# Kernel tuning notes

Hardware: AMD Instinct MI355X
Metric: run time of the kernel (lower is better)

Reference implementation:

```python
import jax, jax.numpy as jnp
import numpy as np

P = 10          # num_patches
EPS = 1e-20
ALPHAS = dict(stretch=1.0, E=1.0, G=1.0, skew=1.0, total_area=1.0, total_area_mult=1.0)
ALPHA_MC = 1.0
ALPHA_DISTORT = 1.0


def setup_inputs() -> dict:
    key = jax.random.key(0)
    k1, k2, k3, k4 = jax.random.split(key, 4)
    B, N, M = 8, 8192, 2500
    pc_gt = jax.random.normal(k1, (B, N, 3), dtype=jnp.float32)
    pc_pred = jax.random.normal(k2, (B, M, 3), dtype=jnp.float32)
    # first fundamental form (E, F, G); ensure E*G - F^2 > 0 so sqrt is smooth
    u = jax.random.uniform(k3, (B, M, 3), dtype=jnp.float32)
    fff = u * 0.5 + jnp.array([1.0, 0.0, 1.0], dtype=jnp.float32)
    A_gt = jax.random.uniform(k4, (B,), dtype=jnp.float32)
    return {"pc_gt": pc_gt, "pc_pred": pc_pred, "fff": fff, "A_gt": A_gt}


def _forward(pc_gt, pc_pred, fff, A_gt):
    B, M, _ = pc_pred.shape
    spp = M // P

    # ---- Chamfer distance via dense (B, M, N) distance matrix + argmin ----
    diff = pc_pred[:, :, None, :] - pc_gt[:, None, :, :]          # (B, M, N, 3)
    distm = jnp.sqrt(jnp.sum(diff * diff, axis=3))                # (B, M, N)
    inds_p2gt = jnp.argmin(distm, axis=2)                         # (B, M)
    inds_gt2p = jnp.argmin(distm, axis=1)                         # (B, N)
    pc_gt_reg = jnp.take_along_axis(pc_gt, inds_p2gt[..., None], axis=1)   # (B, M, 3)
    pc_p_reg = jnp.take_along_axis(pc_pred, inds_gt2p[..., None], axis=1)  # (B, N, 3)
    d_p2gt = jnp.sum((pc_pred - pc_gt_reg) ** 2, axis=2)
    d_gt2p = jnp.sum((pc_gt - pc_p_reg) ** 2, axis=2)
    L_chd = d_p2gt.mean() + d_gt2p.mean()

    # ---- FFF-based losses ----
    EFG = jnp.transpose(fff.reshape(B, P, spp, 3), (3, 0, 1, 2))  # (3, B, P, spp)
    E, F, G = EFG[0], EFG[1], EFG[2]

    # metric consistency between consecutive frame pairs
    Eh = E.reshape(B // 2, 2, P, spp)
    Fh = F.reshape(B // 2, 2, P, spp)
    Gh = G.reshape(B // 2, 2, P, spp)
    L_mc = ((Eh[:, 0] - Eh[:, 1]) ** 2
            + 2.0 * (Fh[:, 0] - Fh[:, 1]) ** 2
            + (Gh[:, 0] - Gh[:, 1]) ** 2).mean()

    # scaled isometry (collapse) losses
    A2 = jnp.maximum(E * G - F * F, 0.0)                          # (B, P, spp)
    A = jnp.sqrt(A2)
    inv = 1.0 / (A2 + EPS)
    L_stretch = (((E - G) ** 2) * inv).mean() * ALPHAS['stretch']
    L_E = (((E - E.mean()) ** 2) * inv).mean() * ALPHAS['E']
    L_G = (((G - G.mean()) ** 2) * inv).mean() * ALPHAS['G']
    L_F = ((F * F) * inv).mean() * ALPHAS['skew']

    # overlap / total-area loss
    A_tot = A.mean(axis=2).sum(axis=1)                            # (B,)
    L_olap = (jnp.maximum(0.0, A_tot - A_gt * ALPHAS['total_area_mult']) ** 2).mean() * ALPHAS['total_area']

    loss_sciso = L_F + L_E + L_G + L_stretch + L_olap
    loss_tot = L_chd + ALPHA_MC * L_mc + ALPHA_DISTORT * loss_sciso
    return loss_tot


def reference(pc_gt, pc_pred, fff, A_gt):
    return _forward(pc_gt, pc_pred, fff, A_gt)
```

## Files before the change

kernel.cpp:

```cpp
#include <hip/hip_runtime.h>

#define B_   8
#define N_   8192
#define M_   2500
#define SPP_ 250
#define EPS_ 1e-20f
#define BIGF 1e30f

#define NB_P2GT 640
#define NB_GT2P 512
#define NB_FFF  79
#define NB_K1   (NB_P2GT + NB_GT2P + NB_FFF)

#define NB_RG2P 256
#define NB_RP2  79
#define NB_K2   (NB_RG2P + NB_RP2)

#define WS_P2GT 0
#define WS_GT2P 160000
#define WS_F1P  291072
#define WS_RED  292968
#define WS_CNT  293303
#define RO_G2P 0
#define RO_P2  256
#define F_E    0
#define F_G    1
#define F_MC   2
#define F_ST   3
#define F_F2I  4
#define F_E2I  5
#define F_EI   6
#define F_G2I  7
#define F_GI   8
#define F_I    9
#define F_AB   10

typedef __attribute__((ext_vector_type(8))) short short8_t;
typedef __attribute__((ext_vector_type(4))) float float4_t;

__device__ __forceinline__ unsigned pack_bf2(float lo, float hi) {
    unsigned a = __float_as_uint(lo);
    unsigned b = __float_as_uint(hi);
    a = (a + 0x7FFFu + ((a >> 16) & 1u)) >> 16;
    b = (b + 0x7FFFu + ((b >> 16) & 1u)) & 0xFFFF0000u;
    return a | b;
}
__device__ __forceinline__ short bf16s(float x) {
    unsigned a = __float_as_uint(x);
    return (short)((a + 0x7FFFu + ((a >> 16) & 1u)) >> 16);
}
__device__ __forceinline__ float wave_sum64(float v) {
    #pragma unroll
    for (int o = 32; o > 0; o >>= 1) v += __shfl_down(v, o, 64);
    return v;
}
__device__ __forceinline__ float block_sum256(float v, volatile float* red4) {
    v = wave_sum64(v);
    int wid = threadIdx.x >> 6, lane = threadIdx.x & 63;
    if (lane == 0) red4[wid] = v;
    __syncthreads();
    float r = 0.f;
    if (threadIdx.x == 0) r = red4[0] + red4[1] + red4[2] + red4[3];
    __syncthreads();
    return r;
}
__device__ __forceinline__ void min4(float4_t& c, const float4_t d) {
    c.x = fminf(c.x, d.x); c.y = fminf(c.y, d.y);
    c.z = fminf(c.z, d.z); c.w = fminf(c.w, d.w);
}
__device__ __forceinline__ void quad_min4(float4_t& c) {
    #pragma unroll
    for (int m = 1; m < 16; m <<= 1) {
        c.x = fminf(c.x, __shfl_xor(c.x, m, 64));
        c.y = fminf(c.y, __shfl_xor(c.y, m, 64));
        c.z = fminf(c.z, __shfl_xor(c.z, m, 64));
        c.w = fminf(c.w, __shfl_xor(c.w, m, 64));
    }
}

__global__ void __launch_bounds__(256, 4) k1_main(
        const float* __restrict__ gt, const float* __restrict__ pred,
        const float* __restrict__ fff, float* __restrict__ ws) {
    __shared__ uint4 spts[1280];
    __shared__ __align__(16) float saux[264];
    const int bid = blockIdx.x;
    const int tid = threadIdx.x;
    const int lane = tid & 63;
    const int w    = tid >> 6;
    const int quad = lane >> 4;
    const int l15  = lane & 15;

    if (bid == 0 && tid == 0) ((unsigned*)(ws + WS_CNT))[0] = 0u;

    if (bid < NB_P2GT + NB_GT2P) {
        const bool is_p2gt = bid < NB_P2GT;
        int b, mblk, z, ntiles, blim, alim;
        const float* apts; const float* bpts; float* dst;
        if (is_p2gt) {
            z = bid / 80; int rem = bid % 80;
            b = rem / 10; mblk = rem % 10;
            apts = pred + (size_t)b * M_ * 3;
            bpts = gt + ((size_t)b * N_ + (size_t)z * 1024) * 3;
            ntiles = 64; blim = 1024; alim = M_;
            dst = ws + WS_P2GT + (size_t)z * 20000 + b * M_;
        } else {
            int r = bid - NB_P2GT;
            z = r >> 8; int rem = r & 255;
            b = rem >> 5; mblk = rem & 31;
            apts = gt + (size_t)b * N_ * 3;
            bpts = pred + ((size_t)b * M_ + (size_t)z * 1280) * 3;
            ntiles = 80; blim = M_ - z * 1280; alim = N_;
            dst = ws + WS_GT2P + (size_t)z * 65536 + b * N_;
        }
        const int abase = mblk * 256;
        const int nstage = ntiles * 16;

        for (int i = tid; i < nstage; i += 256) {
            float x = 0.f, y = 0.f, zc = 0.f, n2 = BIGF;
            if (i < blim) {
                x = bpts[i * 3 + 0]; y = bpts[i * 3 + 1]; zc = bpts[i * 3 + 2];
                n2 = x * x + y * y + zc * zc;
            }
            uint4 q;
            q.x = pack_bf2(-2.f * x, -2.f * y);
            q.y = pack_bf2(-2.f * zc, n2);
            q.z = q.x; q.w = q.y;
            spts[i] = q;
        }

        short8_t af[4];
        #pragma unroll
        for (int t = 0; t < 4; ++t) af[t] = (short8_t){0,0,0,0,0,0,0,0};
        if (lane < 16) {
            #pragma unroll
            for (int t = 0; t < 4; ++t) {
                int m = abase + w * 64 + t * 16 + l15;
                int c = m < alim ? m : alim - 1;
                float x = apts[c*3+0], y = apts[c*3+1], zc = apts[c*3+2];
                af[t][0] = bf16s(x); af[t][1] = bf16s(y); af[t][2] = bf16s(zc);
                af[t][3] = (short)0x3F80;
                saux[w * 64 + t * 16 + l15] = x*x + y*y + zc*zc;
            }
        }
        __syncthreads();

        const float4_t* bp = (const float4_t*)saux;
        float4_t bias[4], c[4];
        #pragma unroll
        for (int t = 0; t < 4; ++t) {
            bias[t] = bp[w * 16 + t * 4 + quad];
            c[t] = (float4_t){BIGF, BIGF, BIGF, BIGF};
        }

        const uint4* bptr = spts + l15;
        const int npairs = ntiles >> 1;
        #pragma unroll 2
        for (int i = 0; i < npairs; ++i) {
            short8_t bf0 = __builtin_bit_cast(short8_t, bptr[(2*i)   * 16]);
            short8_t bf1 = __builtin_bit_cast(short8_t, bptr[(2*i+1) * 16]);
            #pragma unroll
            for (int t = 0; t < 4; ++t) {
                float4_t d = __builtin_amdgcn_mfma_f32_16x16x32_bf16(
                                 af[t], bf0, bias[t], 0, 0, 0);
                min4(c[t], d);
            }
            #pragma unroll
            for (int t = 0; t < 4; ++t) {
                float4_t d = __builtin_amdgcn_mfma_f32_16x16x32_bf16(
                                 af[t], bf1, bias[t], 0, 0, 0);
                min4(c[t], d);
            }
        }
        #pragma unroll
        for (int t = 0; t < 4; ++t) {
            quad_min4(c[t]);
            c[t].x = fmaxf(c[t].x, 0.f); c[t].y = fmaxf(c[t].y, 0.f);
            c[t].z = fmaxf(c[t].z, 0.f); c[t].w = fmaxf(c[t].w, 0.f);
        }
        if (l15 == 0) {
            #pragma unroll
            for (int t = 0; t < 4; ++t) {
                int m0 = abase + w * 64 + t * 16 + quad * 4;
                if (m0 < alim)
                    *(float4_t*)(dst + m0) = c[t];
            }
        }
    } else {
        const int kb = bid - NB_P2GT - NB_GT2P;
        const int i  = kb * 256 + tid;
        volatile float* red4 = saux + 256;
        float* sA = saux;
        if (tid < B_) sA[tid] = 0.f;
        __syncthreads();

        float vE=0.f,vG=0.f,vMC=0.f,vST=0.f,vF2=0.f,vE2=0.f,vEI=0.f,
              vG2=0.f,vGI=0.f,vI=0.f;
        if (i < B_ * M_) {
            const int b = i / M_;
            const int m = i - b * M_;
            const float* f = fff + (size_t)i * 3;
            float E = f[0], F = f[1], G = f[2];
            float A2  = fmaxf(E * G - F * F, 0.f);
            float inv = 1.f / (A2 + EPS_);
            vE = E; vG = G;
            vST = (E - G) * (E - G) * inv;
            vF2 = F * F * inv;
            vE2 = E * E * inv; vEI = E * inv;
            vG2 = G * G * inv; vGI = G * inv;
            vI  = inv;
            atomicAdd(&sA[b], sqrtf(A2));
            if ((b & 1) == 0) {
                const float* f2 = fff + ((size_t)(b + 1) * M_ + m) * 3;
                float dE = E - f2[0], dF = F - f2[1], dG = G - f2[2];
                vMC = dE * dE + 2.f * dF * dF + dG * dG;
            }
        }
        float* outp = ws + WS_F1P + (size_t)kb * 24;
        float r;
        r = block_sum256(vE,  red4); if (tid==0) outp[F_E]   = r;
        r = block_sum256(vG,  red4); if (tid==0) outp[F_G]   = r;
        r = block_sum256(vMC, red4); if (tid==0) outp[F_MC]  = r;
        r = block_sum256(vST, red4); if (tid==0) outp[F_ST]  = r;
        r = block_sum256(vF2, red4); if (tid==0) outp[F_F2I] = r;
        r = block_sum256(vE2, red4); if (tid==0) outp[F_E2I] = r;
        r = block_sum256(vEI, red4); if (tid==0) outp[F_EI]  = r;
        r = block_sum256(vG2, red4); if (tid==0) outp[F_G2I] = r;
        r = block_sum256(vGI, red4); if (tid==0) outp[F_GI]  = r;
        r = block_sum256(vI,  red4); if (tid==0) outp[F_I]   = r;
        __syncthreads();
        if (tid < B_) outp[F_AB + tid] = sA[tid];
    }
}

__global__ void __launch_bounds__(256) k2_reduce(
        const float* __restrict__ fff, const float* __restrict__ A_gt,
        float* __restrict__ ws, float* __restrict__ out) {
    __shared__ float red4[4];
    const int bid = blockIdx.x;
    const int tid = threadIdx.x;
    float* redp = ws + WS_RED;
    const float* f1p = ws + WS_F1P;

    if (bid < NB_RG2P) {
        const int o = bid * 256 + tid;
        const float* src = ws + WS_GT2P + o;
        float m = fminf(src[0], src[65536]);
        float r = block_sum256(m, red4);
        if (tid == 0) redp[RO_G2P + bid] = r;
    } else {
        const int kb = bid - NB_RG2P;
        const int o = kb * 256 + tid;
        float s = 0.f;
        if (o < 20000) {
            const float* src = ws + WS_P2GT + o;
            float m = src[0];
            #pragma unroll
            for (int zz = 1; zz < 8; ++zz) m = fminf(m, src[zz * 20000]);
            s = m;
        }
        float r = block_sum256(s, red4);
        if (tid == 0) redp[RO_P2 + kb] = r;
    }

    __syncthreads();
    if (tid == 0) __threadfence();
    __syncthreads();
    __shared__ unsigned old_s;
    if (tid == 0)
        old_s = __hip_atomic_fetch_add((unsigned*)(ws + WS_CNT), 1u,
                                       __ATOMIC_ACQ_REL, __HIP_MEMORY_SCOPE_AGENT);
    __syncthreads();
    if (old_s == (unsigned)(NB_K2 - 1)) {
        float v;
        v = redp[RO_G2P + tid];
        float sGT2P = block_sum256(v, red4);
        v = (tid < 79) ? redp[RO_P2 + tid] : 0.f;
        float sP2GT = block_sum256(v, red4);
        float a[18];
        #pragma unroll
        for (int k = 0; k < 18; ++k) {
            v = (tid < 79) ? f1p[tid * 24 + k] : 0.f;
            a[k] = block_sum256(v, red4);
        }
        if (tid == 0) {
            const float inv20k = 1.f / 20000.f;
            float mE = a[F_E] * inv20k, mG = a[F_G] * inv20k;
            float L_E = (a[F_E2I] - 2.f*mE*a[F_EI] + mE*mE*a[F_I]) * inv20k;
            float L_G = (a[F_G2I] - 2.f*mG*a[F_GI] + mG*mG*a[F_I]) * inv20k;
            float L_sc = L_E + L_G + (a[F_ST] + a[F_F2I]) * inv20k;
            float L_mc = a[F_MC] * (1.f / 10000.f);
            float L_chd = sP2GT * inv20k + sGT2P * (1.f / 65536.f);
            float L_olap = 0.f;
            #pragma unroll
            for (int b = 0; b < B_; ++b) {
                float At = a[F_AB + b] * (1.f / (float)SPP_);
                float d  = fmaxf(0.f, At - A_gt[b]);
                L_olap += d * d;
            }
            L_olap *= (1.f / (float)B_);
            out[0] = L_chd + L_mc + L_sc + L_olap;
        }
    }
}

extern "C" void kernel_launch(void* const* d_in, const int* in_sizes, int n_in,
                              void* d_out, int out_size, void* d_ws, size_t ws_size,
                              hipStream_t stream) {
    const float* pc_gt   = (const float*)d_in[0];
    const float* pc_pred = (const float*)d_in[1];
    const float* fff     = (const float*)d_in[2];
    const float* A_gt    = (const float*)d_in[3];
    float* ws  = (float*)d_ws;
    float* out = (float*)d_out;

    k1_main  <<<NB_K1, 256, 0, stream>>>(pc_gt, pc_pred, fff, ws);
    k2_reduce<<<NB_K2, 256, 0, stream>>>(fff, A_gt, ws, out);
}
```

Measured before the change: 100.9 us.

## Enlarge Chamfer MFMA tiles and fuse gt2p min-sum into main kernel

Each block now processes 512 query points (8 MFMA tiles per wave) instead of 256. The gt-to-pred direction covers all predicted points in one block, so it no longer needs a split over two chunks. That direction now reduces the per-point minima to a per-block sum inside the main kernel rather than writing a 65536x2 intermediate, and the reduce kernel drops its 256 gt2p blocks. The intent is to raise data reuse per LDS load and cut global traffic and reduction work. In exchange, LDS use and register pressure roughly double, occupancy falls (launch bounds 4 to 2), and the gt2p phase has only 128 blocks, which risks underfilling the GPU.

```diff
diff --git a/kernel.cpp b/kernel.cpp
--- a/kernel.cpp
+++ b/kernel.cpp
@@ -7,22 +7,18 @@
 #define EPS_ 1e-20f
 #define BIGF 1e30f
 
-#define NB_P2GT 640
-#define NB_GT2P 512
+#define NB_P2GT 320
+#define NB_GT2P 128
 #define NB_FFF  79
 #define NB_K1   (NB_P2GT + NB_GT2P + NB_FFF)
 
-#define NB_RG2P 256
-#define NB_RP2  79
-#define NB_K2   (NB_RG2P + NB_RP2)
+#define NB_K2   79
 
 #define WS_P2GT 0
-#define WS_GT2P 160000
-#define WS_F1P  291072
-#define WS_RED  292968
-#define WS_CNT  293303
-#define RO_G2P 0
-#define RO_P2  256
+#define WS_G2PS 160000
+#define WS_F1P  160128
+#define WS_RED  162024
+#define WS_CNT  162103
 #define F_E    0
 #define F_G    1
 #define F_MC   2
@@ -78,11 +74,11 @@
     }
 }
 
-__global__ void __launch_bounds__(256, 4) k1_main(
+__global__ void __launch_bounds__(256, 2) k1_main(
         const float* __restrict__ gt, const float* __restrict__ pred,
         const float* __restrict__ fff, float* __restrict__ ws) {
-    __shared__ uint4 spts[1280];
-    __shared__ __align__(16) float saux[264];
+    __shared__ uint4 spts[2512];
+    __shared__ __align__(16) float saux[520];
     const int bid = blockIdx.x;
     const int tid = threadIdx.x;
     const int lane = tid & 63;
@@ -94,25 +90,23 @@
 
     if (bid < NB_P2GT + NB_GT2P) {
         const bool is_p2gt = bid < NB_P2GT;
-        int b, mblk, z, ntiles, blim, alim;
-        const float* apts; const float* bpts; float* dst;
+        int b, mblk, ntiles, blim, alim;
+        const float* apts; const float* bpts; float* dst = nullptr;
         if (is_p2gt) {
-            z = bid / 80; int rem = bid % 80;
-            b = rem / 10; mblk = rem % 10;
+            int z = bid / 40; int rem = bid % 40;
+            b = rem / 5;  mblk = rem % 5;
             apts = pred + (size_t)b * M_ * 3;
             bpts = gt + ((size_t)b * N_ + (size_t)z * 1024) * 3;
             ntiles = 64; blim = 1024; alim = M_;
             dst = ws + WS_P2GT + (size_t)z * 20000 + b * M_;
         } else {
             int r = bid - NB_P2GT;
-            z = r >> 8; int rem = r & 255;
-            b = rem >> 5; mblk = rem & 31;
+            b = r >> 4; mblk = r & 15;
             apts = gt + (size_t)b * N_ * 3;
-            bpts = pred + ((size_t)b * M_ + (size_t)z * 1280) * 3;
-            ntiles = 80; blim = M_ - z * 1280; alim = N_;
-            dst = ws + WS_GT2P + (size_t)z * 65536 + b * N_;
-        }
-        const int abase = mblk * 256;
+            bpts = pred + (size_t)b * M_ * 3;
+            ntiles = 157; blim = M_; alim = N_;
+        }
+        const int abase = mblk * 512;
         const int nstage = ntiles * 16;
 
         for (int i = tid; i < nstage; i += 256) {
@@ -128,67 +122,75 @@
             spts[i] = q;
         }
 
-        short8_t af[4];
+        short8_t af[8];
         #pragma unroll
-        for (int t = 0; t < 4; ++t) af[t] = (short8_t){0,0,0,0,0,0,0,0};
+        for (int t = 0; t < 8; ++t) af[t] = (short8_t){0,0,0,0,0,0,0,0};
         if (lane < 16) {
             #pragma unroll
-            for (int t = 0; t < 4; ++t) {
-                int m = abase + w * 64 + t * 16 + l15;
+            for (int t = 0; t < 8; ++t) {
+                int m = abase + w * 128 + t * 16 + l15;
                 int c = m < alim ? m : alim - 1;
                 float x = apts[c*3+0], y = apts[c*3+1], zc = apts[c*3+2];
                 af[t][0] = bf16s(x); af[t][1] = bf16s(y); af[t][2] = bf16s(zc);
                 af[t][3] = (short)0x3F80;
-                saux[w * 64 + t * 16 + l15] = x*x + y*y + zc*zc;
+                saux[w * 128 + t * 16 + l15] = x*x + y*y + zc*zc;
             }
         }
         __syncthreads();
 
         const float4_t* bp = (const float4_t*)saux;
-        float4_t bias[4], c[4];
+        float4_t bias[8], c[8];
         #pragma unroll
-        for (int t = 0; t < 4; ++t) {
-            bias[t] = bp[w * 16 + t * 4 + quad];
+        for (int t = 0; t < 8; ++t) {
+            bias[t] = bp[w * 32 + t * 4 + quad];
             c[t] = (float4_t){BIGF, BIGF, BIGF, BIGF};
         }
 
         const uint4* bptr = spts + l15;
-        const int npairs = ntiles >> 1;
         #pragma unroll 2
-        for (int i = 0; i < npairs; ++i) {
-            short8_t bf0 = __builtin_bit_cast(short8_t, bptr[(2*i)   * 16]);
-            short8_t bf1 = __builtin_bit_cast(short8_t, bptr[(2*i+1) * 16]);
+        for (int i = 0; i < ntiles; ++i) {
+            short8_t bf = __builtin_bit_cast(short8_t, bptr[i * 16]);
             #pragma unroll
-            for (int t = 0; t < 4; ++t) {
+            for (int t = 0; t < 8; ++t) {
                 float4_t d = __builtin_amdgcn_mfma_f32_16x16x32_bf16(
-                                 af[t], bf0, bias[t], 0, 0, 0);
+                                 af[t], bf, bias[t], 0, 0, 0);
                 min4(c[t], d);
             }
-            #pragma unroll
-            for (int t = 0; t < 4; ++t) {
-                float4_t d = __builtin_amdgcn_mfma_f32_16x16x32_bf16(
-                                 af[t], bf1, bias[t], 0, 0, 0);
-                min4(c[t], d);
-            }
         }
         #pragma unroll
-        for (int t = 0; t < 4; ++t) {
+        for (int t = 0; t < 8; ++t) {
             quad_min4(c[t]);
             c[t].x = fmaxf(c[t].x, 0.f); c[t].y = fmaxf(c[t].y, 0.f);
             c[t].z = fmaxf(c[t].z, 0.f); c[t].w = fmaxf(c[t].w, 0.f);
         }
-        if (l15 == 0) {
-            #pragma unroll
-            for (int t = 0; t < 4; ++t) {
-                int m0 = abase + w * 64 + t * 16 + quad * 4;
-                if (m0 < alim)
-                    *(float4_t*)(dst + m0) = c[t];
-            }
+
+        if (is_p2gt) {
+            if (l15 == 0) {
+                #pragma unroll
+                for (int t = 0; t < 8; ++t) {
+                    int m0 = abase + w * 128 + t * 16 + quad * 4;
+                    if (m0 < alim)
+                        *(float4_t*)(dst + m0) = c[t];
+                }
+            }
+        } else {
+            float s = 0.f;
+            if (l15 == 0) {
+                #pragma unroll
+                for (int t = 0; t < 8; ++t)
+                    s += c[t].x + c[t].y + c[t].z + c[t].w;
+            }
+            s = wave_sum64(s);
+            if (lane == 0) saux[512 + w] = s;
+            __syncthreads();
+            if (tid == 0)
+                ws[WS_G2PS + (bid - NB_P2GT)] =
+                    saux[512] + saux[513] + saux[514] + saux[515];
         }
     } else {
         const int kb = bid - NB_P2GT - NB_GT2P;
         const int i  = kb * 256 + tid;
-        volatile float* red4 = saux + 256;
+        volatile float* red4 = saux + 512;
         float* sA = saux;
         if (tid < B_) sA[tid] = 0.f;
         __syncthreads();
@@ -241,15 +243,8 @@
     float* redp = ws + WS_RED;
     const float* f1p = ws + WS_F1P;
 
-    if (bid < NB_RG2P) {
+    {
         const int o = bid * 256 + tid;
-        const float* src = ws + WS_GT2P + o;
-        float m = fminf(src[0], src[65536]);
-        float r = block_sum256(m, red4);
-        if (tid == 0) redp[RO_G2P + bid] = r;
-    } else {
-        const int kb = bid - NB_RG2P;
-        const int o = kb * 256 + tid;
         float s = 0.f;
         if (o < 20000) {
             const float* src = ws + WS_P2GT + o;
@@ -259,7 +254,7 @@
             s = m;
         }
         float r = block_sum256(s, red4);
-        if (tid == 0) redp[RO_P2 + kb] = r;
+        if (tid == 0) redp[bid] = r;
     }
 
     __syncthreads();
@@ -272,10 +267,10 @@
     __syncthreads();
     if (old_s == (unsigned)(NB_K2 - 1)) {
         float v;
-        v = redp[RO_G2P + tid];
+        v = (tid < NB_K2) ? redp[tid] : 0.f;
+        float sP2GT = block_sum256(v, red4);
+        v = (tid < 128) ? ws[WS_G2PS + tid] : 0.f;
         float sGT2P = block_sum256(v, red4);
-        v = (tid < 79) ? redp[RO_P2 + tid] : 0.f;
-        float sP2GT = block_sum256(v, red4);
         float a[18];
         #pragma unroll
         for (int k = 0; k < 18; ++k) {
```

New measurement: 125.7 us. 1.25x slower.
